# Optimization experiments

Hardware: AMD Instinct MI355X
Metric: run time of the kernel (lower is better)

The kernel has to match this reference:

```python
import jax, jax.numpy as jnp
import numpy as np

B, S, D = 16, 2048, 128

def setup_inputs() -> dict:
    key = jax.random.key(0)
    k1, k2, k3 = jax.random.split(key, 3)
    return {
        "query": jax.random.normal(k1, (B, S, D), dtype=jnp.float32),
        "key": jax.random.normal(k2, (B, S, D), dtype=jnp.float32),
        "value": jax.random.normal(k3, (B, S, D), dtype=jnp.float32),
    }

def reference(query, key, value):
    dq = query.shape[-1]
    dk = key.shape[-1]
    # custom scale: sqrt(Dq) + sqrt(Dk - Dq); with Dq == Dk this is sqrt(Dq)
    inv_scale = np.sqrt(dq) + np.sqrt(dk - dq)
    qk = jnp.einsum("bqd,bkd->bqk", query, key) / jnp.float32(inv_scale)
    attn = jax.nn.softmax(qk, axis=-1)  # dropout_p=0 -> identity
    return jnp.einsum("bqk,bkd->bqd", attn, value)
```

## Files before the change

kernel.cpp:

```cpp
#include <hip/hip_runtime.h>
#include <stdint.h>

#define Bn 16
#define Sn 2048
#define Dn 128
#define QBLK 64
#define KVBLK 64
#define NTHR 256
#define NT (Sn / KVBLK)

typedef __attribute__((ext_vector_type(4))) float f32x4;
typedef __attribute__((ext_vector_type(16))) float f32x16;
typedef __attribute__((ext_vector_type(8))) short bf16x8;
typedef __attribute__((ext_vector_type(2))) unsigned int u32x2;

#define SMEM_BYTES 33792

__device__ __forceinline__ uint32_t f2bf_u(float f) {
  return (__float_as_uint(f) + 0x8000u) >> 16;
}
__device__ __forceinline__ uint32_t pk2(float a, float b) {
  return f2bf_u(a) | (f2bf_u(b) << 16);
}

__global__ __launch_bounds__(256) void tr_kv(const float* __restrict__ K,
                                             const float* __restrict__ V,
                                             unsigned short* __restrict__ Kf,
                                             unsigned short* __restrict__ Vf) {
  __shared__ unsigned short lds[64 * 136];
  const int tid = threadIdx.x;
  const size_t tileoff = (size_t)blockIdx.x * (64 * Dn);

  {
    const float* src = K + tileoff;
#pragma unroll
    for (int it = 0; it < 8; ++it) {
      const int gr = it * 256 + tid;
      const int k = gr >> 5, g4 = gr & 31;
      const float4 v = ((const float4*)src)[gr];
      unsigned short* p = &lds[k * 136 + g4 * 4];
      p[0] = (unsigned short)f2bf_u(v.x);
      p[1] = (unsigned short)f2bf_u(v.y);
      p[2] = (unsigned short)f2bf_u(v.z);
      p[3] = (unsigned short)f2bf_u(v.w);
    }
    __syncthreads();
    char* dst = (char*)Kf + (size_t)blockIdx.x * 16384;
#pragma unroll
    for (int it = 0; it < 4; ++it) {
      const int g = it * 256 + tid;
      const int lane = g & 63, dk = (g >> 6) & 7, h = g >> 9;
      const unsigned short* p =
          &lds[(32 * h + (lane & 31)) * 136 + dk * 16 + 8 * (lane >> 5)];
      uint4 o;
      o.x = (uint32_t)p[0] | ((uint32_t)p[1] << 16);
      o.y = (uint32_t)p[2] | ((uint32_t)p[3] << 16);
      o.z = (uint32_t)p[4] | ((uint32_t)p[5] << 16);
      o.w = (uint32_t)p[6] | ((uint32_t)p[7] << 16);
      *(uint4*)(dst + g * 16) = o;
    }
  }
  __syncthreads();

  {
    const float* src = V + tileoff;
#pragma unroll
    for (int it = 0; it < 8; ++it) {
      const int gr = it * 256 + tid;
      const int k = gr >> 5, g4 = gr & 31;
      const float4 v = ((const float4*)src)[gr];
      unsigned short* p = &lds[k * 136 + g4 * 4];
      p[0] = (unsigned short)f2bf_u(v.x);
      p[1] = (unsigned short)f2bf_u(v.y);
      p[2] = (unsigned short)f2bf_u(v.z);
      p[3] = (unsigned short)f2bf_u(v.w);
    }
    __syncthreads();
    char* dst = (char*)Vf + (size_t)blockIdx.x * 16384;
#pragma unroll
    for (int it = 0; it < 4; ++it) {
      const int g = it * 256 + tid;
      const int lane = g & 63, f3 = (g >> 6) & 7, h = g >> 9;
      const int d = (f3 >> 1) * 32 + (lane & 31);
      const int k0 = 32 * h + (f3 & 1) * 16 + 8 * (lane >> 5);
      uint4 o;
      o.x = (uint32_t)lds[(k0 + 0) * 136 + d] | ((uint32_t)lds[(k0 + 1) * 136 + d] << 16);
      o.y = (uint32_t)lds[(k0 + 2) * 136 + d] | ((uint32_t)lds[(k0 + 3) * 136 + d] << 16);
      o.z = (uint32_t)lds[(k0 + 4) * 136 + d] | ((uint32_t)lds[(k0 + 5) * 136 + d] << 16);
      o.w = (uint32_t)lds[(k0 + 6) * 136 + d] | ((uint32_t)lds[(k0 + 7) * 136 + d] << 16);
      *(uint4*)(dst + g * 16) = o;
    }
  }
}

__global__ __launch_bounds__(NTHR, 2) void attn_fwd(
    const float* __restrict__ Q, const unsigned short* __restrict__ Kf,
    const unsigned short* __restrict__ Vf, float* __restrict__ O) {
  __shared__ uint4 smem_[SMEM_BYTES / 16];
  char* smem = (char*)smem_;

  const int tid = threadIdx.x;
  const int lane = tid & 63;
  const int w = tid >> 6;
  const int qw = w & 1;
  const int h = w >> 1;
  const int hi = lane >> 5;
  const int ql = lane & 31;

  const int i = blockIdx.x;
  const int j = i >> 3;
  const int b = (i & 7) + 8 * (j & 1);
  const int q0 = (j >> 1) * QBLK;
  const int qg = q0 + qw * 32 + ql;

  const float qscale = 0.08838834764831845f * 1.44269504088896340736f;
  bf16x8 qf[8];
  {
    const float* qrow = Q + (size_t)(b * Sn + qg) * Dn;
#pragma unroll
    for (int dk = 0; dk < 8; ++dk) {
      const int d0 = dk * 16 + hi * 8;
      const float4 a = *(const float4*)(qrow + d0);
      const float4 d = *(const float4*)(qrow + d0 + 4);
      bf16x8 q8;
      q8[0] = (short)f2bf_u(a.x * qscale); q8[1] = (short)f2bf_u(a.y * qscale);
      q8[2] = (short)f2bf_u(a.z * qscale); q8[3] = (short)f2bf_u(a.w * qscale);
      q8[4] = (short)f2bf_u(d.x * qscale); q8[5] = (short)f2bf_u(d.y * qscale);
      q8[6] = (short)f2bf_u(d.z * qscale); q8[7] = (short)f2bf_u(d.w * qscale);
      qf[dk] = q8;
    }
  }

  f32x16 o[4];
#pragma unroll
  for (int dt = 0; dt < 4; ++dt) {
#pragma unroll
    for (int jj = 0; jj < 16; ++jj) o[dt][jj] = 0.f;
  }
  float m_r = -1.0e30f, l_r = 0.f;

  const char* Kg = (const char*)(Kf + (size_t)b * Sn * Dn);
  const char* Vg = (const char*)(Vf + (size_t)b * Sn * Dn);

#define LOADK(kd_, t_)                                                         \
  {                                                                            \
    const char* kt = Kg + (size_t)(t_)*16384 + h * 8192 + lane * 16;           \
    _Pragma("unroll") for (int f = 0; f < 8; ++f)                              \
        kd_[f] = *(const bf16x8*)(kt + f * 1024);                              \
  }

#define TILE(kf_, t_)                                                          \
  {                                                                            \
    bf16x8 vfr[8];                                                             \
    {                                                                          \
      const char* vt = Vg + (size_t)(t_)*16384 + h * 8192 + lane * 16;         \
      _Pragma("unroll") for (int f = 0; f < 8; ++f)                            \
          vfr[f] = *(const bf16x8*)(vt + f * 1024);                            \
    }                                                                          \
    f32x16 s;                                                                  \
    _Pragma("unroll") for (int jj = 0; jj < 16; ++jj) s[jj] = 0.f;             \
    __builtin_amdgcn_s_setprio(1);                                             \
    _Pragma("unroll") for (int dk = 0; dk < 8; ++dk)                           \
        s = __builtin_amdgcn_mfma_f32_32x32x16_bf16(kf_[dk], qf[dk], s, 0, 0, 0);\
    __builtin_amdgcn_s_setprio(0);                                             \
    float x0 = fmaxf(fmaxf(s[0], s[1]), fmaxf(s[2], s[3]));                    \
    float x1 = fmaxf(fmaxf(s[4], s[5]), fmaxf(s[6], s[7]));                    \
    float x2 = fmaxf(fmaxf(s[8], s[9]), fmaxf(s[10], s[11]));                  \
    float x3 = fmaxf(fmaxf(s[12], s[13]), fmaxf(s[14], s[15]));                \
    float pm = fmaxf(fmaxf(x0, x1), fmaxf(x2, x3));                            \
    pm = fmaxf(pm, __shfl_xor(pm, 32, 64));                                    \
    if (!__all(pm <= m_r + 8.0f)) {                       \
      const float mnew = fmaxf(m_r, pm);                                       \
      const float alpha = __builtin_amdgcn_exp2f(m_r - mnew);                  \
      l_r *= alpha;                                                            \
      _Pragma("unroll") for (int dt = 0; dt < 4; ++dt) o[dt] *= alpha;         \
      m_r = mnew;                                                              \
    }                                                                          \
    _Pragma("unroll") for (int jj = 0; jj < 16; ++jj)                          \
        s[jj] = __builtin_amdgcn_exp2f(s[jj] - m_r);                           \
    {                                                                          \
      float r0 = 0.f, r1 = 0.f, r2 = 0.f, r3 = 0.f;                            \
      _Pragma("unroll") for (int jj = 0; jj < 4; ++jj) {                       \
        r0 += s[jj]; r1 += s[4 + jj]; r2 += s[8 + jj]; r3 += s[12 + jj];       \
      }                                                                        \
      l_r += (r0 + r1) + (r2 + r3);      \
    }                                                                          \
    uint32_t own[4][2];                                                        \
    _Pragma("unroll") for (int mm = 0; mm < 4; ++mm) {                         \
      own[mm][0] = pk2(s[4 * mm + 0], s[4 * mm + 1]);                          \
      own[mm][1] = pk2(s[4 * mm + 2], s[4 * mm + 3]);                          \
    }                                                                          \
    uint32_t rcv[2][2];                                                        \
    _Pragma("unroll") for (int jj = 0; jj < 2; ++jj)                           \
        _Pragma("unroll") for (int e = 0; e < 2; ++e) {                        \
      uint32_t sel = hi ? own[2 * jj][e] : own[2 * jj + 1][e];                 \
      rcv[jj][e] = (uint32_t)__shfl_xor((int)sel, 32, 64);                     \
    }                                                                          \
    bf16x8 pb[2];                                                              \
    _Pragma("unroll") for (int ks = 0; ks < 2; ++ks) {                         \
      union { uint32_t u[4]; bf16x8 v; } tt;                                   \
      tt.u[0] = hi ? rcv[ks][0] : own[2 * ks][0];                              \
      tt.u[1] = hi ? rcv[ks][1] : own[2 * ks][1];                              \
      tt.u[2] = hi ? own[2 * ks + 1][0] : rcv[ks][0];                          \
      tt.u[3] = hi ? own[2 * ks + 1][1] : rcv[ks][1];                          \
      pb[ks] = tt.v;                                                           \
    }                                                                          \
    __builtin_amdgcn_s_setprio(1);                                             \
    _Pragma("unroll") for (int dt = 0; dt < 4; ++dt) {                         \
      _Pragma("unroll") for (int ks = 0; ks < 2; ++ks) {                       \
        o[dt] = __builtin_amdgcn_mfma_f32_32x32x16_bf16(vfr[dt * 2 + ks],      \
                                                        pb[ks], o[dt], 0, 0, 0);\
      }                                                                        \
    }                                                                          \
    __builtin_amdgcn_s_setprio(0);                                             \
  }

  bf16x8 kC[8], kN[8];
  LOADK(kC, 0)
  __builtin_amdgcn_sched_barrier(0);
  for (int t = 0; t < NT; t += 2) {
    LOADK(kN, t + 1)
    __builtin_amdgcn_sched_barrier(0);
    TILE(kC, t)
    if (t + 2 < NT) {
      LOADK(kC, t + 2)
    }
    __builtin_amdgcn_sched_barrier(0);
    TILE(kN, t + 1)
  }

  l_r += __shfl_xor(l_r, 32, 64);
  __syncthreads();
  char* xch = smem + qw * 16896;
  if (h) {
#pragma unroll
    for (int dt = 0; dt < 4; ++dt) {
#pragma unroll
      for (int q2 = 0; q2 < 4; ++q2) {
        float4 v;
        v.x = o[dt][4 * q2 + 0]; v.y = o[dt][4 * q2 + 1];
        v.z = o[dt][4 * q2 + 2]; v.w = o[dt][4 * q2 + 3];
        *(float4*)(xch + (dt * 4 + q2) * 1024 + lane * 16) = v;
      }
    }
    *(float2*)(xch + 16384 + lane * 8) = make_float2(m_r, l_r);
  }
  __syncthreads();
  if (!h) {
    const float2 ml1v = *(const float2*)(xch + 16384 + lane * 8);
    const float M = fmaxf(m_r, ml1v.x);
    const float w0 = __builtin_amdgcn_exp2f(m_r - M);
    const float w1 = __builtin_amdgcn_exp2f(ml1v.x - M);
    const float inv = 1.0f / (l_r * w0 + ml1v.y * w1);
    const float s0 = w0 * inv, s1 = w1 * inv;
    float* orow = O + (size_t)(b * Sn + qg) * Dn;
#pragma unroll
    for (int dt = 0; dt < 4; ++dt) {
#pragma unroll
      for (int q2 = 0; q2 < 4; ++q2) {
        const float4 o1v =
            *(const float4*)(xch + (dt * 4 + q2) * 1024 + lane * 16);
        float4 v;
        v.x = o[dt][4 * q2 + 0] * s0 + o1v.x * s1;
        v.y = o[dt][4 * q2 + 1] * s0 + o1v.y * s1;
        v.z = o[dt][4 * q2 + 2] * s0 + o1v.z * s1;
        v.w = o[dt][4 * q2 + 3] * s0 + o1v.w * s1;
        *(float4*)(orow + dt * 32 + q2 * 8 + hi * 4) = v;
      }
    }
  }
}

extern "C" void kernel_launch(void* const* d_in, const int* in_sizes, int n_in,
                              void* d_out, int out_size, void* d_ws, size_t ws_size,
                              hipStream_t stream) {
  (void)in_sizes; (void)n_in; (void)out_size; (void)ws_size;
  const float* Q = (const float*)d_in[0];
  const float* K = (const float*)d_in[1];
  const float* V = (const float*)d_in[2];
  float* O = (float*)d_out;

  const size_t nE = (size_t)Bn * Sn * Dn;
  unsigned short* Kf = (unsigned short*)d_ws;
  unsigned short* Vf = Kf + nE;

  tr_kv<<<dim3(Bn * 32, 1, 1), dim3(256, 1, 1), 0, stream>>>(K, V, Kf, Vf);
  attn_fwd<<<dim3((Sn / QBLK) * Bn, 1, 1), dim3(NTHR, 1, 1), 0, stream>>>(
      Q, Kf, Vf, O);
}
```

Baseline: 64.11 us.

## Software-pipeline QK^T of the next tile against softmax and PV of the current

Splits the per-tile body into separate QK^T, softmax+PV, and V-load stages. The QK^T MFMAs for tile t+1 are now issued before the softmax and PV of tile t, so matrix work can overlap the exp/shuffle VALU work. K is double-buffered two tiles ahead. This costs an extra 16-float score accumulator per lane and more register pressure, which could reduce occupancy.

```diff
diff --git a/kernel.cpp b/kernel.cpp
--- a/kernel.cpp
+++ b/kernel.cpp
@@ -148,25 +148,28 @@
     _Pragma("unroll") for (int f = 0; f < 8; ++f)                              \
         kd_[f] = *(const bf16x8*)(kt + f * 1024);                              \
   }
-
-#define TILE(kf_, t_)                                                          \
-  {                                                                            \
-    bf16x8 vfr[8];                                                             \
-    {                                                                          \
-      const char* vt = Vg + (size_t)(t_)*16384 + h * 8192 + lane * 16;         \
-      _Pragma("unroll") for (int f = 0; f < 8; ++f)                            \
-          vfr[f] = *(const bf16x8*)(vt + f * 1024);                            \
-    }                                                                          \
-    f32x16 s;                                                                  \
-    _Pragma("unroll") for (int jj = 0; jj < 16; ++jj) s[jj] = 0.f;             \
+#define LOADV(vd_, t_)                                                         \
+  {                                                                            \
+    const char* vt = Vg + (size_t)(t_)*16384 + h * 8192 + lane * 16;           \
+    _Pragma("unroll") for (int f = 0; f < 8; ++f)                              \
+        vd_[f] = *(const bf16x8*)(vt + f * 1024);                              \
+  }
+
+#define QKT(sd_, kf_)                                                          \
+  {                                                                            \
+    _Pragma("unroll") for (int jj = 0; jj < 16; ++jj) sd_[jj] = 0.f;           \
     __builtin_amdgcn_s_setprio(1);                                             \
     _Pragma("unroll") for (int dk = 0; dk < 8; ++dk)                           \
-        s = __builtin_amdgcn_mfma_f32_32x32x16_bf16(kf_[dk], qf[dk], s, 0, 0, 0);\
+        sd_ = __builtin_amdgcn_mfma_f32_32x32x16_bf16(kf_[dk], qf[dk], sd_, 0, 0, 0);\
     __builtin_amdgcn_s_setprio(0);                                             \
-    float x0 = fmaxf(fmaxf(s[0], s[1]), fmaxf(s[2], s[3]));                    \
-    float x1 = fmaxf(fmaxf(s[4], s[5]), fmaxf(s[6], s[7]));                    \
-    float x2 = fmaxf(fmaxf(s[8], s[9]), fmaxf(s[10], s[11]));                  \
-    float x3 = fmaxf(fmaxf(s[12], s[13]), fmaxf(s[14], s[15]));                \
+  }
+
+#define SOFTPV(s_, vf_)                                                        \
+  {                                                                            \
+    float x0 = fmaxf(fmaxf(s_[0], s_[1]), fmaxf(s_[2], s_[3]));                \
+    float x1 = fmaxf(fmaxf(s_[4], s_[5]), fmaxf(s_[6], s_[7]));                \
+    float x2 = fmaxf(fmaxf(s_[8], s_[9]), fmaxf(s_[10], s_[11]));              \
+    float x3 = fmaxf(fmaxf(s_[12], s_[13]), fmaxf(s_[14], s_[15]));            \
     float pm = fmaxf(fmaxf(x0, x1), fmaxf(x2, x3));                            \
     pm = fmaxf(pm, __shfl_xor(pm, 32, 64));                                    \
     if (!__all(pm <= m_r + 8.0f)) {                       \
@@ -177,18 +180,18 @@
       m_r = mnew;                                                              \
     }                                                                          \
     _Pragma("unroll") for (int jj = 0; jj < 16; ++jj)                          \
-        s[jj] = __builtin_amdgcn_exp2f(s[jj] - m_r);                           \
+        s_[jj] = __builtin_amdgcn_exp2f(s_[jj] - m_r);                         \
     {                                                                          \
       float r0 = 0.f, r1 = 0.f, r2 = 0.f, r3 = 0.f;                            \
       _Pragma("unroll") for (int jj = 0; jj < 4; ++jj) {                       \
-        r0 += s[jj]; r1 += s[4 + jj]; r2 += s[8 + jj]; r3 += s[12 + jj];       \
+        r0 += s_[jj]; r1 += s_[4 + jj]; r2 += s_[8 + jj]; r3 += s_[12 + jj];   \
       }                                                                        \
       l_r += (r0 + r1) + (r2 + r3);      \
     }                                                                          \
     uint32_t own[4][2];                                                        \
     _Pragma("unroll") for (int mm = 0; mm < 4; ++mm) {                         \
-      own[mm][0] = pk2(s[4 * mm + 0], s[4 * mm + 1]);                          \
-      own[mm][1] = pk2(s[4 * mm + 2], s[4 * mm + 3]);                          \
+      own[mm][0] = pk2(s_[4 * mm + 0], s_[4 * mm + 1]);                        \
+      own[mm][1] = pk2(s_[4 * mm + 2], s_[4 * mm + 3]);                        \
     }                                                                          \
     uint32_t rcv[2][2];                                                        \
     _Pragma("unroll") for (int jj = 0; jj < 2; ++jj)                           \
@@ -208,25 +211,30 @@
     __builtin_amdgcn_s_setprio(1);                                             \
     _Pragma("unroll") for (int dt = 0; dt < 4; ++dt) {                         \
       _Pragma("unroll") for (int ks = 0; ks < 2; ++ks) {                       \
-        o[dt] = __builtin_amdgcn_mfma_f32_32x32x16_bf16(vfr[dt * 2 + ks],      \
+        o[dt] = __builtin_amdgcn_mfma_f32_32x32x16_bf16(vf_[dt * 2 + ks],      \
                                                         pb[ks], o[dt], 0, 0, 0);\
       }                                                                        \
     }                                                                          \
     __builtin_amdgcn_s_setprio(0);                                             \
   }
 
-  bf16x8 kC[8], kN[8];
-  LOADK(kC, 0)
+  bf16x8 kA[8], kB[8], vC[8];
+  f32x16 s0, s1;
+  LOADK(kA, 0)
+  LOADK(kB, 1)
   __builtin_amdgcn_sched_barrier(0);
+  QKT(s0, kA)
   for (int t = 0; t < NT; t += 2) {
-    LOADK(kN, t + 1)
+    LOADV(vC, t)
+    if (t + 2 < NT) LOADK(kA, t + 2)
     __builtin_amdgcn_sched_barrier(0);
-    TILE(kC, t)
-    if (t + 2 < NT) {
-      LOADK(kC, t + 2)
-    }
+    QKT(s1, kB)
+    SOFTPV(s0, vC)
+    LOADV(vC, t + 1)
+    if (t + 3 < NT) LOADK(kB, t + 3)
     __builtin_amdgcn_sched_barrier(0);
-    TILE(kN, t + 1)
+    if (t + 2 < NT) QKT(s0, kA)
+    SOFTPV(s1, vC)
   }
 
   l_r += __shfl_xor(l_r, 32, 64);
@@ -252,7 +260,7 @@
     const float w0 = __builtin_amdgcn_exp2f(m_r - M);
     const float w1 = __builtin_amdgcn_exp2f(ml1v.x - M);
     const float inv = 1.0f / (l_r * w0 + ml1v.y * w1);
-    const float s0 = w0 * inv, s1 = w1 * inv;
+    const float s0v = w0 * inv, s1v = w1 * inv;
     float* orow = O + (size_t)(b * Sn + qg) * Dn;
 #pragma unroll
     for (int dt = 0; dt < 4; ++dt) {
@@ -261,10 +269,10 @@
         const float4 o1v =
             *(const float4*)(xch + (dt * 4 + q2) * 1024 + lane * 16);
         float4 v;
-        v.x = o[dt][4 * q2 + 0] * s0 + o1v.x * s1;
-        v.y = o[dt][4 * q2 + 1] * s0 + o1v.y * s1;
-        v.z = o[dt][4 * q2 + 2] * s0 + o1v.z * s1;
-        v.w = o[dt][4 * q2 + 3] * s0 + o1v.w * s1;
+        v.x = o[dt][4 * q2 + 0] * s0v + o1v.x * s1v;
+        v.y = o[dt][4 * q2 + 1] * s0v + o1v.y * s1v;
+        v.z = o[dt][4 * q2 + 2] * s0v + o1v.z * s1v;
+        v.w = o[dt][4 * q2 + 3] * s0v + o1v.w * s1v;
         *(float4*)(orow + dt * 32 + q2 * 8 + hi * 4) = v;
       }
     }
```

Result: no change. 65.30 us (+1.9%).
